# Kernel optimization log

Hardware: AMD Instinct MI355X
Metric: run time of the kernel (lower is better)

## Reference

```python
import jax, jax.numpy as jnp
import numpy as np

B, M, D = 8, 1024, 1024
H = 16
HD = D // H  # 64
F = 4096

def layer_norm(x, gamma, beta, eps=1e-5):
    mu = jnp.mean(x, axis=-1, keepdims=True)
    var = jnp.var(x, axis=-1, keepdims=True)
    return (x - mu) * jax.lax.rsqrt(var + eps) * gamma + beta

def setup_inputs() -> dict:
    key = jax.random.key(0)
    ks = jax.random.split(key, 16)
    s = 0.02
    return {
        "h": jax.random.normal(ks[0], (B, M, D), jnp.float32),
        "h_all": jax.random.normal(ks[1], (B, M, D), jnp.float32),
        "Wq": jax.random.normal(ks[2], (D, D), jnp.float32) * s,
        "Wk": jax.random.normal(ks[3], (D, D), jnp.float32) * s,
        "Wv": jax.random.normal(ks[4], (D, D), jnp.float32) * s,
        "Wo": jax.random.normal(ks[5], (D, D), jnp.float32) * s,
        "W1": jax.random.normal(ks[6], (D, F), jnp.float32) * s,
        "b1": jnp.zeros((F,), jnp.float32),
        "W2": jax.random.normal(ks[7], (F, D), jnp.float32) * s,
        "b2": jnp.zeros((D,), jnp.float32),
        "g1": jnp.ones((D,), jnp.float32),
        "be1": jnp.zeros((D,), jnp.float32),
        "g2": jnp.ones((D,), jnp.float32),
        "be2": jnp.zeros((D,), jnp.float32),
    }

def reference(h, h_all, Wq, Wk, Wv, Wo, W1, b1, W2, b2, g1, be1, g2, be2):
    Bx, Mx, Dx = h.shape
    # projections (no bias, per nn.Linear(bias=False))
    q = (h @ Wq).reshape(Bx, Mx, H, HD)        # [B,M,H,hd]
    k = (h_all @ Wk).reshape(Bx, -1, H, HD)    # [B,N,H,hd]
    v = (h_all @ Wv).reshape(Bx, -1, H, HD)
    # attention: scale by sqrt(head_dim) as in SeqAttention(hidden_size=head_dim)
    scores = jnp.einsum('bqhd,bkhd->bhqk', q, k) / jnp.sqrt(jnp.float32(HD))
    attn = jax.nn.softmax(scores, axis=-1)
    ctx = jnp.einsum('bhqk,bkhd->bqhd', attn, v).reshape(Bx, Mx, Dx)
    attn_out = ctx @ Wo
    # post-norm residual 1
    h1 = layer_norm(h + attn_out, g1, be1)
    # FFN
    ff = jax.nn.relu(h1 @ W1 + b1) @ W2 + b2
    # post-norm residual 2
    out = layer_norm(h1 + ff, g2, be2)
    return out
```

## Files before the change

kernel.cpp:

```cpp
#include <hip/hip_runtime.h>
#include <hip/hip_bf16.h>

#define ROWS 8192
#define DD   1024
#define HH   16
#define HD   64
#define FF   4096

typedef __attribute__((ext_vector_type(4))) float f32x4;
typedef __attribute__((ext_vector_type(8))) __bf16 bf16x8;

static __device__ __forceinline__ unsigned short f2bf(float f) {
  unsigned u = __float_as_uint(f);
  u += 0x7fffu + ((u >> 16) & 1u);
  return (unsigned short)(u >> 16);
}

static __device__ __forceinline__ float bf2f(unsigned short u) {
  return __uint_as_float(((unsigned)u) << 16);
}

static __device__ __forceinline__ unsigned cvtpk_bf16(float lo, float hi) {
  unsigned r;
  asm("v_cvt_pk_bf16_f32 %0, %1, %2" : "=v"(r) : "v"(lo), "v"(hi));
  return r;
}

static __device__ __forceinline__ f32x4 mfma16(bf16x8 a, bf16x8 b, f32x4 c) {
  return __builtin_amdgcn_mfma_f32_16x16x32_bf16(a, b, c, 0, 0, 0);
}

#define GLOAD16(gp, lp) __builtin_amdgcn_global_load_lds( \
    (__attribute__((address_space(1))) void*)(gp), \
    (__attribute__((address_space(3))) void*)(lp), 16, 0, 0)

__global__ __launch_bounds__(256) void prep_k(
    const float* __restrict__ h, const float* __restrict__ hall,
    const float* __restrict__ Wq, const float* __restrict__ Wk,
    const float* __restrict__ Wv, const float* __restrict__ Wo,
    const float* __restrict__ W1, const float* __restrict__ W2,
    unsigned short* __restrict__ hb, unsigned short* __restrict__ hab,
    unsigned short* __restrict__ wqt, unsigned short* __restrict__ wkvt,
    unsigned short* __restrict__ wot, unsigned short* __restrict__ w1t,
    unsigned short* __restrict__ w2t) {
  __shared__ float tile[32][33];
  const int bid = blockIdx.x;
  const int tid = threadIdx.x;

  if (bid < 16384) {
    const float* src = (bid < 8192) ? h : hall;
    unsigned short* dst = (bid < 8192) ? hb : hab;
    int i = (bid & 8191) * 256 + tid;
    float4 v = ((const float4*)src)[i];
    ushort4 o;
    o.x = f2bf(v.x); o.y = f2bf(v.y); o.z = f2bf(v.z); o.w = f2bf(v.w);
    ((ushort4*)dst)[i] = o;
    return;
  }

  int r = bid - 16384;
  const float* src; unsigned short* dst; int R, C, bx, by;
  if (r < 4096) {
    int which = r >> 10, idx = r & 1023;
    R = C = 1024; bx = idx & 31; by = idx >> 5;
    if (which == 0) { src = Wq; dst = wqt; }
    else if (which == 1) { src = Wk; dst = wkvt; }
    else if (which == 2) { src = Wv; dst = wkvt + (size_t)DD * DD; }
    else { src = Wo; dst = wot; }
  } else if (r < 8192) {
    int idx = r - 4096;
    R = 1024; C = 4096; bx = idx & 127; by = idx >> 7;
    src = W1; dst = w1t;
  } else {
    int idx = r - 8192;
    R = 4096; C = 1024; bx = idx & 31; by = idx >> 5;
    src = W2; dst = w2t;
  }
  const int tx = tid & 31, ty = tid >> 5;
  #pragma unroll
  for (int i = 0; i < 32; i += 8)
    tile[ty + i][tx] = src[(size_t)(by * 32 + ty + i) * C + bx * 32 + tx];
  __syncthreads();
  #pragma unroll
  for (int i = 0; i < 32; i += 8)
    dst[(size_t)(bx * 32 + ty + i) * R + by * 32 + tx] = f2bf(tile[tx][ty + i]);
}

template <int BM, int MODE, int KS = 1>
__global__ __launch_bounds__(512, 2) void gemm256(
    const unsigned short* __restrict__ A, const unsigned short* __restrict__ BT,
    const float* __restrict__ bias, void* __restrict__ Cout, void* __restrict__ Cout2,
    int Ni, int Ki, int nbx) {
  constexpr int MR = BM / 32;

  const int tid  = threadIdx.x;
  const int lane = tid & 63;
  const int wid  = tid >> 6;
  const int wm   = wid >> 2;
  const int wn   = wid & 3;
  const int lr   = lane & 15;
  const int kq   = lane >> 4;
  const int axor = (lr & 7) << 4;

  const int nwg = gridDim.x;
  const int cpx = nwg >> 3;
  const int wg  = (int)blockIdx.x;
  const int swz = (wg & 7) * cpx + (wg >> 3);
  const int perk = nwg / KS;
  const int kh   = swz / perk;
  const int swzr = swz % perk;
  const int bx = swzr % nbx, by = swzr / nbx;
  const int brow = by * BM, bcol = bx * 256;
  const int Kc   = Ki / KS;
  const int kbase = kh * Kc;

  f32x4 acc[MR][4] = {};
  const int NT = Kc >> 6;

  if constexpr (BM == 256) {
    __shared__ unsigned short As[2 * 256 * 64];
    __shared__ unsigned short Bs[2 * 256 * 64];

    const size_t loff = (size_t)(lane >> 3) * Ki + ((lane & 7) ^ (lane >> 3)) * 8;
    const unsigned short* Ab = A + (size_t)brow * Ki + kbase;
    const unsigned short* Bb = BT + (size_t)bcol * Ki + kbase;

    auto stage2 = [&](int qc, int u, int db) {
      const int ra = ((wid & 4) << 5) + qc * 32 + (wid & 3) * 8;
      GLOAD16(Ab + (size_t)ra * Ki + u * 64 + loff,
              (char*)As + db * 32768 + ra * 128);
      const int rb = qc * 64 + wid * 8;
      GLOAD16(Bb + (size_t)rb * Ki + u * 64 + loff,
              (char*)Bs + db * 32768 + rb * 128);
    };

    #pragma unroll
    for (int qc = 0; qc < 4; ++qc) stage2(qc, 0, 0);
    {
      const int u1 = (1 < NT) ? 1 : NT - 1;
      stage2(0, u1, 1); stage2(1, u1, 1); stage2(2, u1, 1);
    }
    asm volatile("s_waitcnt vmcnt(6)" ::: "memory");
    __builtin_amdgcn_s_barrier();
    __builtin_amdgcn_sched_barrier(0);

    #pragma unroll 1
    for (int t = 0; t < NT; ++t) {
      const int d = t & 1;
      const char* ab = (const char*)As + d * 32768;
      const char* bb = (const char*)Bs + d * 32768;
      bf16x8 bfv[4][2];
      #pragma unroll
      for (int q = 0; q < 4; ++q) {
        bf16x8 af[2][2];
        #pragma unroll
        for (int mm = 0; mm < 2; ++mm)
          #pragma unroll
          for (int ks = 0; ks < 2; ++ks)
            af[mm][ks] = *(const bf16x8*)(ab +
                (wm * 128 + (q * 2 + mm) * 16 + lr) * 128 +
                ((ks * 64 + kq * 16) ^ axor));
        if (q == 0) {
          #pragma unroll
          for (int n = 0; n < 4; ++n)
            #pragma unroll
            for (int ks = 0; ks < 2; ++ks)
              bfv[n][ks] = *(const bf16x8*)(bb +
                  (wn * 64 + n * 16 + lr) * 128 +
                  ((ks * 64 + kq * 16) ^ axor));
        }
        if (q == 0) {
          stage2(3, (t + 1 < NT) ? t + 1 : NT - 1, (t + 1) & 1);
        } else {
          stage2(q - 1, (t + 2 < NT) ? t + 2 : NT - 1, d);
        }
        __builtin_amdgcn_s_setprio(1);
        #pragma unroll
        for (int mm = 0; mm < 2; ++mm)
          #pragma unroll
          for (int n = 0; n < 4; ++n) {
            acc[q * 2 + mm][n] = mfma16(af[mm][0], bfv[n][0], acc[q * 2 + mm][n]);
            acc[q * 2 + mm][n] = mfma16(af[mm][1], bfv[n][1], acc[q * 2 + mm][n]);
          }
        __builtin_amdgcn_s_setprio(0);
        __builtin_amdgcn_sched_barrier(0);
        if (q == 3) asm volatile("s_waitcnt vmcnt(6)" ::: "memory");
        __builtin_amdgcn_s_barrier();
        __builtin_amdgcn_sched_barrier(0);
      }
    }
    asm volatile("s_waitcnt vmcnt(0)" ::: "memory");
  } else {
    __shared__ unsigned short As[2][BM * 64];
    __shared__ unsigned short Bs[2][256 * 64];
    const int srow = wid * 8 + (lane >> 3);
    const int scol = ((lane & 7) * 8) ^ ((srow & 7) << 3);
    size_t offA[BM / 64], offB[4];
    #pragma unroll
    for (int L = 0; L < BM / 64; ++L)
      offA[L] = (size_t)(brow + L * 64 + srow) * Ki + kbase + scol;
    #pragma unroll
    for (int L = 0; L < 4; ++L)
      offB[L] = (size_t)(bcol + L * 64 + srow) * Ki + kbase + scol;

    auto stage = [&](int t, int d) {
      #pragma unroll
      for (int L = 0; L < BM / 64; ++L)
        GLOAD16(A + offA[L] + t * 64, (char*)As[d] + L * 8192 + wid * 1024);
      #pragma unroll
      for (int L = 0; L < 4; ++L)
        GLOAD16(BT + offB[L] + t * 64, (char*)Bs[d] + L * 8192 + wid * 1024);
    };

    stage(0, 0);
    stage(1, 1);

    #pragma unroll 1
    for (int t = 0; t < NT; ++t) {
      const int d = t & 1;
      asm volatile("s_waitcnt vmcnt(6)" ::: "memory");
      __builtin_amdgcn_s_barrier();
      __builtin_amdgcn_sched_barrier(0);

      const unsigned short* as = As[d];
      const unsigned short* bs = Bs[d];
      #pragma unroll
      for (int kk = 0; kk < 2; ++kk) {
        bf16x8 af[MR], bfv[4];
        #pragma unroll
        for (int m = 0; m < MR; ++m)
          af[m] = *(const bf16x8*)((const char*)as +
              (wm * (BM / 2) + m * 16 + lr) * 128 + ((kk * 64 + kq * 16) ^ axor));
        #pragma unroll
        for (int n = 0; n < 4; ++n)
          bfv[n] = *(const bf16x8*)((const char*)bs +
              (wn * 64 + n * 16 + lr) * 128 + ((kk * 64 + kq * 16) ^ axor));
        #pragma unroll
        for (int m = 0; m < MR; ++m)
          #pragma unroll
          for (int n = 0; n < 4; ++n)
            acc[m][n] = mfma16(af[m], bfv[n], acc[m][n]);
      }

      asm volatile("s_waitcnt lgkmcnt(0)" ::: "memory");
      __builtin_amdgcn_s_barrier();
      __builtin_amdgcn_sched_barrier(0);
      const int ts = (t + 2 < NT) ? t + 2 : NT - 1;
      stage(ts, d);
    }
  }

  #pragma unroll
  for (int m = 0; m < MR; ++m) {
    #pragma unroll
    for (int n = 0; n < 4; ++n) {
      const int r0 = brow + wm * (BM / 2) + m * 16 + kq * 4;
      const int c  = bcol + wn * 64 + n * 16 + lr;
      if constexpr (MODE == 4) {
        if (c < 1024) {
          #pragma unroll
          for (int e = 0; e < 4; ++e)
            ((unsigned short*)Cout)[(size_t)(r0 + e) * 1024 + c] = f2bf(acc[m][n][e]);
        } else {
          const int cc = c - 1024;
          const int bq = r0 >> 10;
          const int tok = r0 & 1023;
          ushort4 pk;
          pk.x = f2bf(acc[m][n][0]); pk.y = f2bf(acc[m][n][1]);
          pk.z = f2bf(acc[m][n][2]); pk.w = f2bf(acc[m][n][3]);
          *(ushort4*)((unsigned short*)Cout2 + ((size_t)bq * 1024 + cc) * 1024 + tok) = pk;
        }
      } else if constexpr (MODE == 5) {
        unsigned short* o = (kh == 0) ? (unsigned short*)Cout : (unsigned short*)Cout2;
        #pragma unroll
        for (int e = 0; e < 4; ++e)
          o[(size_t)(r0 + e) * Ni + c] = f2bf(acc[m][n][e]);
      } else {
        const float bv = (MODE == 2 || MODE == 3) ? bias[c] : 0.0f;
        #pragma unroll
        for (int e = 0; e < 4; ++e) {
          float v = acc[m][n][e] + bv;
          if (MODE == 2) v = fmaxf(v, 0.0f);
          if (MODE == 0 || MODE == 2)
            ((unsigned short*)Cout)[(size_t)(r0 + e) * Ni + c] = f2bf(v);
          else
            ((float*)Cout)[(size_t)(r0 + e) * Ni + c] = v;
        }
      }
    }
  }
}

__global__ __launch_bounds__(512, 6) void attn_k(
    const unsigned short* __restrict__ q, const unsigned short* __restrict__ k,
    const unsigned short* __restrict__ vT, unsigned short* __restrict__ ctx) {
  __shared__ unsigned short Ks[2][64 * 64];
  __shared__ unsigned short Vt[2][64 * 64];
  __shared__ unsigned short Ps[8][16 * 64];
  const int tid = threadIdx.x;
  const int lane = tid & 63;
  const int wid = tid >> 6;
  const int bh = blockIdx.x;
  const int b = bh >> 4, h = bh & 15;
  const int qrow0 = blockIdx.y * 128 + wid * 16;
  const size_t tokbase = (size_t)b * 1024;
  const int lr = lane & 15, kq = lane >> 4;

  const int srow = tid >> 3;
  const int scol = ((tid & 7) * 8) ^ ((srow & 7) << 3);
  const unsigned short* kg = k + (tokbase + srow) * 1024 + h * 64 + scol;
  const unsigned short* vg = vT + ((size_t)(b * 16 + h) * 64 + srow) * 1024 + scol;
  const int ldst = tid * 16;

  auto stage = [&](int kt, int d) {
    GLOAD16(kg + (size_t)kt * 64 * 1024, (char*)Ks[d] + ldst);
    GLOAD16(vg + kt * 64, (char*)Vt[d] + ldst);
  };

  bf16x8 aq[2];
  {
    const unsigned short* qp = q + (tokbase + qrow0 + lr) * DD + h * 64 + kq * 8;
    aq[0] = *(const bf16x8*)qp;
    aq[1] = *(const bf16x8*)(qp + 32);
  }

  float l_acc = 0.f;
  f32x4 acc[4] = {};
  const float C = 0.125f * 1.4426950408889634f;
  const unsigned swp = (unsigned)((lr & 7) << 4);
  const unsigned pbase = (unsigned)(lr * 128);

  stage(0, 0);
  stage(1, 1);

  #pragma unroll 2
  for (int kt = 0; kt < 16; ++kt) {
    const int d = kt & 1;
    asm volatile("s_waitcnt vmcnt(2)" ::: "memory");
    __builtin_amdgcn_s_barrier();
    __builtin_amdgcn_sched_barrier(0);

    f32x4 sv[4] = {};
    __builtin_amdgcn_s_setprio(1);
    #pragma unroll
    for (int jb = 0; jb < 4; ++jb)
      #pragma unroll
      for (int ks = 0; ks < 2; ++ks) {
        int row = jb * 16 + lr;
        bf16x8 ak = *(const bf16x8*)((const char*)Ks[d] +
            row * 128 + ((ks * 64 + kq * 16) ^ ((row & 7) << 4)));
        sv[jb] = mfma16(ak, aq[ks], sv[jb]);
      }
    __builtin_amdgcn_s_setprio(0);

    #pragma unroll
    for (int jb = 0; jb < 4; ++jb) {
      float p0 = exp2f(sv[jb][0] * C);
      float p1 = exp2f(sv[jb][1] * C);
      float p2 = exp2f(sv[jb][2] * C);
      float p3 = exp2f(sv[jb][3] * C);
      l_acc += (p0 + p1) + (p2 + p3);
      uint2 w;
      w.x = cvtpk_bf16(p0, p1);
      w.y = cvtpk_bf16(p2, p3);
      unsigned off = pbase + (((unsigned)(jb * 32 + kq * 8)) ^ swp);
      *(uint2*)((char*)Ps[wid] + off) = w;
    }

    __builtin_amdgcn_s_setprio(1);
    #pragma unroll
    for (int ks = 0; ks < 2; ++ks) {
      bf16x8 ap = *(const bf16x8*)((const char*)Ps[wid] +
          lr * 128 + ((ks * 64 + kq * 16) ^ ((lr & 7) << 4)));
      #pragma unroll
      for (int db = 0; db < 4; ++db) {
        int dd = db * 16 + lr;
        bf16x8 bv = *(const bf16x8*)((const char*)Vt[d] +
            dd * 128 + ((ks * 64 + kq * 16) ^ ((dd & 7) << 4)));
        acc[db] = mfma16(bv, ap, acc[db]);
      }
    }
    __builtin_amdgcn_s_setprio(0);

    asm volatile("s_waitcnt lgkmcnt(0)" ::: "memory");
    __builtin_amdgcn_s_barrier();
    __builtin_amdgcn_sched_barrier(0);
    const int ts = (kt + 2 < 16) ? kt + 2 : 15;
    stage(ts, d);
  }

  float l = l_acc + __shfl_xor(l_acc, 16);
  l += __shfl_xor(l, 32);
  const float inv = 1.0f / l;
  unsigned short* cp = ctx + (tokbase + qrow0 + lr) * DD + h * 64 + kq * 4;
  #pragma unroll
  for (int db = 0; db < 4; ++db) {
    ushort4 o;
    o.x = f2bf(acc[db][0] * inv);
    o.y = f2bf(acc[db][1] * inv);
    o.z = f2bf(acc[db][2] * inv);
    o.w = f2bf(acc[db][3] * inv);
    *(ushort4*)(cp + db * 16) = o;
  }
}

__global__ __launch_bounds__(256) void ln_add_bb_k(
    const unsigned short* __restrict__ a, const unsigned short* __restrict__ b,
    const float* __restrict__ gamma, const float* __restrict__ beta,
    unsigned short* __restrict__ outb) {
  int row = blockIdx.x;
  int tid = threadIdx.x;
  size_t base = (size_t)row * 1024 + tid * 4;
  ushort4 va = *(const ushort4*)(a + base);
  ushort4 vb = *(const ushort4*)(b + base);
  float x[4] = {bf2f(va.x) + bf2f(vb.x), bf2f(va.y) + bf2f(vb.y),
                bf2f(va.z) + bf2f(vb.z), bf2f(va.w) + bf2f(vb.w)};
  float s = x[0] + x[1] + x[2] + x[3];
  float sq = x[0] * x[0] + x[1] * x[1] + x[2] * x[2] + x[3] * x[3];
  #pragma unroll
  for (int mk = 1; mk < 64; mk <<= 1) {
    s += __shfl_xor(s, mk);
    sq += __shfl_xor(sq, mk);
  }
  __shared__ float red[8];
  int wid = tid >> 6, lane = tid & 63;
  if (lane == 0) { red[wid] = s; red[4 + wid] = sq; }
  __syncthreads();
  s = red[0] + red[1] + red[2] + red[3];
  sq = red[4] + red[5] + red[6] + red[7];
  float mu = s * (1.0f / 1024.0f);
  float var = sq * (1.0f / 1024.0f) - mu * mu;
  float rs = rsqrtf(var + 1e-5f);
  float4 g = *(const float4*)(gamma + tid * 4);
  float4 be = *(const float4*)(beta + tid * 4);
  ushort4 ob;
  ob.x = f2bf((x[0] - mu) * rs * g.x + be.x);
  ob.y = f2bf((x[1] - mu) * rs * g.y + be.y);
  ob.z = f2bf((x[2] - mu) * rs * g.z + be.z);
  ob.w = f2bf((x[3] - mu) * rs * g.w + be.w);
  *(ushort4*)(outb + base) = ob;
}

__global__ __launch_bounds__(256) void ln3_k(
    const unsigned short* __restrict__ a, const unsigned short* __restrict__ p0,
    const unsigned short* __restrict__ p1, const float* __restrict__ b2,
    const float* __restrict__ gamma, const float* __restrict__ beta,
    float* __restrict__ outf) {
  int row = blockIdx.x;
  int tid = threadIdx.x;
  size_t base = (size_t)row * 1024 + tid * 4;
  ushort4 va = *(const ushort4*)(a + base);
  ushort4 v0 = *(const ushort4*)(p0 + base);
  ushort4 v1 = *(const ushort4*)(p1 + base);
  float4 bb = *(const float4*)(b2 + tid * 4);
  float x[4] = {bf2f(va.x) + bf2f(v0.x) + bf2f(v1.x) + bb.x,
                bf2f(va.y) + bf2f(v0.y) + bf2f(v1.y) + bb.y,
                bf2f(va.z) + bf2f(v0.z) + bf2f(v1.z) + bb.z,
                bf2f(va.w) + bf2f(v0.w) + bf2f(v1.w) + bb.w};
  float s = x[0] + x[1] + x[2] + x[3];
  float sq = x[0] * x[0] + x[1] * x[1] + x[2] * x[2] + x[3] * x[3];
  #pragma unroll
  for (int mk = 1; mk < 64; mk <<= 1) {
    s += __shfl_xor(s, mk);
    sq += __shfl_xor(sq, mk);
  }
  __shared__ float red[8];
  int wid = tid >> 6, lane = tid & 63;
  if (lane == 0) { red[wid] = s; red[4 + wid] = sq; }
  __syncthreads();
  s = red[0] + red[1] + red[2] + red[3];
  sq = red[4] + red[5] + red[6] + red[7];
  float mu = s * (1.0f / 1024.0f);
  float var = sq * (1.0f / 1024.0f) - mu * mu;
  float rs = rsqrtf(var + 1e-5f);
  float4 g = *(const float4*)(gamma + tid * 4);
  float4 be = *(const float4*)(beta + tid * 4);
  float4 o;
  o.x = (x[0] - mu) * rs * g.x + be.x;
  o.y = (x[1] - mu) * rs * g.y + be.y;
  o.z = (x[2] - mu) * rs * g.z + be.z;
  o.w = (x[3] - mu) * rs * g.w + be.w;
  *(float4*)(outf + base) = o;
}

extern "C" void kernel_launch(void* const* d_in, const int* in_sizes, int n_in,
                              void* d_out, int out_size, void* d_ws, size_t ws_size,
                              hipStream_t stream) {
  const float* h    = (const float*)d_in[0];
  const float* hall = (const float*)d_in[1];
  const float* Wq   = (const float*)d_in[2];
  const float* Wk   = (const float*)d_in[3];
  const float* Wv   = (const float*)d_in[4];
  const float* Wo   = (const float*)d_in[5];
  const float* W1   = (const float*)d_in[6];
  const float* b1   = (const float*)d_in[7];
  const float* W2   = (const float*)d_in[8];
  const float* b2   = (const float*)d_in[9];
  const float* g1   = (const float*)d_in[10];
  const float* be1  = (const float*)d_in[11];
  const float* g2   = (const float*)d_in[12];
  const float* be2  = (const float*)d_in[13];

  char* ws = (char*)d_ws;
  size_t off = 0;
  auto alloc = [&](size_t n) { size_t o = off; off += (n + 255) & ~(size_t)255; return o; };
  const size_t hb_o   = alloc((size_t)ROWS * DD * 2);
  const size_t hab_o  = alloc((size_t)ROWS * DD * 2);
  const size_t wqt_o  = alloc((size_t)DD * DD * 2);
  const size_t wkvt_o = alloc((size_t)DD * DD * 4);
  const size_t wot_o  = alloc((size_t)DD * DD * 2);
  const size_t w1t_o  = alloc((size_t)DD * FF * 2);
  const size_t w2t_o  = alloc((size_t)FF * DD * 2);
  const size_t qb_o   = alloc((size_t)ROWS * DD * 2);
  const size_t kb_o   = alloc((size_t)ROWS * DD * 2);
  const size_t vt_o   = alloc((size_t)ROWS * DD * 2);
  const size_t cx_o   = alloc((size_t)ROWS * DD * 2);
  const size_t h1b_o  = alloc((size_t)ROWS * DD * 2);
  const size_t fp1_o  = alloc((size_t)ROWS * DD * 2);

  unsigned short* hb   = (unsigned short*)(ws + hb_o);
  unsigned short* hab  = (unsigned short*)(ws + hab_o);
  unsigned short* wqt  = (unsigned short*)(ws + wqt_o);
  unsigned short* wkvt = (unsigned short*)(ws + wkvt_o);
  unsigned short* wot  = (unsigned short*)(ws + wot_o);
  unsigned short* w1t  = (unsigned short*)(ws + w1t_o);
  unsigned short* w2t  = (unsigned short*)(ws + w2t_o);
  unsigned short* qb   = (unsigned short*)(ws + qb_o);
  unsigned short* kb   = (unsigned short*)(ws + kb_o);
  unsigned short* vTb  = (unsigned short*)(ws + vt_o);
  unsigned short* cxb  = (unsigned short*)(ws + cx_o);
  unsigned short* h1b  = (unsigned short*)(ws + h1b_o);
  unsigned short* fp1b = (unsigned short*)(ws + fp1_o);
  unsigned short* attn_ob = (unsigned short*)(ws + hab_o);
  unsigned short* fp0b    = (unsigned short*)(ws + hb_o);
  unsigned short* ff1     = (unsigned short*)(ws + qb_o);
  float*          outf    = (float*)d_out;

  prep_k<<<dim3(16384 + 4096 + 4096 + 4096), 256, 0, stream>>>(
      h, hall, Wq, Wk, Wv, Wo, W1, W2, hb, hab, wqt, wkvt, wot, w1t, w2t);

  gemm256<128, 0><<<dim3(256), 512, 0, stream>>>(hb,  wqt,  nullptr, qb, nullptr, DD,   DD, 4);
  gemm256<256, 4><<<dim3(256), 512, 0, stream>>>(hab, wkvt, nullptr, kb, vTb,    2048, DD, 8);

  attn_k<<<dim3(128, 8), 512, 0, stream>>>(qb, kb, vTb, cxb);

  gemm256<128, 0><<<dim3(256), 512, 0, stream>>>(cxb, wot, nullptr, attn_ob, nullptr, DD, DD, 4);
  ln_add_bb_k<<<ROWS, 256, 0, stream>>>(hb, attn_ob, g1, be1, h1b);

  gemm256<256, 2>   <<<dim3(512), 512, 0, stream>>>(h1b, w1t, b1, ff1, nullptr, FF, DD, 16);
  gemm256<256, 5, 2><<<dim3(256), 512, 0, stream>>>(ff1, w2t, nullptr, fp0b, fp1b, DD, FF, 4);

  ln3_k<<<ROWS, 256, 0, stream>>>(h1b, fp0b, fp1b, b2, g2, be2, outf);
}
```

Baseline: 342.9 us.

## Merge Q and KV projection GEMMs into one launch and widen transpose tiles

The Q projection and the fused K/V projection GEMMs now run as a single 512-block launch. The GEMM body is factored into a device function that takes the LDS buffers and the block index as arguments, so the two GEMMs of different shapes share one kernel and fill the GPU together instead of running back to back. Separately, the weight-transpose prep now uses 64x64 tiles, converting to bf16 before the data goes to shared memory, which means fewer blocks and a smaller LDS footprint per element. The merged kernel reserves a full 128KB of LDS for every block, including the BM=128 ones, and the wider tiles change the store pattern.

```diff
diff --git a/kernel.cpp b/kernel.cpp
--- a/kernel.cpp
+++ b/kernel.cpp
@@ -43,7 +43,7 @@
     unsigned short* __restrict__ wqt, unsigned short* __restrict__ wkvt,
     unsigned short* __restrict__ wot, unsigned short* __restrict__ w1t,
     unsigned short* __restrict__ w2t) {
-  __shared__ float tile[32][33];
+  __shared__ unsigned short tile[64][66];
   const int bid = blockIdx.x;
   const int tid = threadIdx.x;
 
@@ -60,37 +60,42 @@
 
   int r = bid - 16384;
   const float* src; unsigned short* dst; int R, C, bx, by;
-  if (r < 4096) {
-    int which = r >> 10, idx = r & 1023;
-    R = C = 1024; bx = idx & 31; by = idx >> 5;
+  if (r < 1024) {
+    int which = r >> 8, idx = r & 255;
+    R = C = 1024; bx = idx & 15; by = idx >> 4;
     if (which == 0) { src = Wq; dst = wqt; }
     else if (which == 1) { src = Wk; dst = wkvt; }
     else if (which == 2) { src = Wv; dst = wkvt + (size_t)DD * DD; }
     else { src = Wo; dst = wot; }
-  } else if (r < 8192) {
-    int idx = r - 4096;
-    R = 1024; C = 4096; bx = idx & 127; by = idx >> 7;
+  } else if (r < 2048) {
+    int idx = r - 1024;
+    R = 1024; C = 4096; bx = idx & 63; by = idx >> 6;
     src = W1; dst = w1t;
   } else {
-    int idx = r - 8192;
-    R = 4096; C = 1024; bx = idx & 31; by = idx >> 5;
+    int idx = r - 2048;
+    R = 4096; C = 1024; bx = idx & 15; by = idx >> 4;
     src = W2; dst = w2t;
   }
-  const int tx = tid & 31, ty = tid >> 5;
+  const int col = tid & 63, q4 = tid >> 6;
   #pragma unroll
-  for (int i = 0; i < 32; i += 8)
-    tile[ty + i][tx] = src[(size_t)(by * 32 + ty + i) * C + bx * 32 + tx];
+  for (int i = 0; i < 16; ++i) {
+    int rr = q4 + i * 4;
+    tile[rr][col] = f2bf(src[(size_t)(by * 64 + rr) * C + bx * 64 + col]);
+  }
   __syncthreads();
   #pragma unroll
-  for (int i = 0; i < 32; i += 8)
-    dst[(size_t)(bx * 32 + ty + i) * R + by * 32 + tx] = f2bf(tile[tx][ty + i]);
+  for (int i = 0; i < 16; ++i) {
+    int c = q4 + i * 4;
+    dst[(size_t)(bx * 64 + c) * R + by * 64 + col] = tile[col][c];
+  }
 }
 
 template <int BM, int MODE, int KS = 1>
-__global__ __launch_bounds__(512, 2) void gemm256(
+static __device__ __forceinline__ void gemm_body(
+    char* ldsA, char* ldsB,
     const unsigned short* __restrict__ A, const unsigned short* __restrict__ BT,
     const float* __restrict__ bias, void* __restrict__ Cout, void* __restrict__ Cout2,
-    int Ni, int Ki, int nbx) {
+    int Ni, int Ki, int nbx, int wg, int nwg) {
   constexpr int MR = BM / 32;
 
   const int tid  = threadIdx.x;
@@ -102,9 +107,7 @@
   const int kq   = lane >> 4;
   const int axor = (lr & 7) << 4;
 
-  const int nwg = gridDim.x;
   const int cpx = nwg >> 3;
-  const int wg  = (int)blockIdx.x;
   const int swz = (wg & 7) * cpx + (wg >> 3);
   const int perk = nwg / KS;
   const int kh   = swz / perk;
@@ -118,20 +121,15 @@
   const int NT = Kc >> 6;
 
   if constexpr (BM == 256) {
-    __shared__ unsigned short As[2 * 256 * 64];
-    __shared__ unsigned short Bs[2 * 256 * 64];
-
     const size_t loff = (size_t)(lane >> 3) * Ki + ((lane & 7) ^ (lane >> 3)) * 8;
     const unsigned short* Ab = A + (size_t)brow * Ki + kbase;
     const unsigned short* Bb = BT + (size_t)bcol * Ki + kbase;
 
     auto stage2 = [&](int qc, int u, int db) {
       const int ra = ((wid & 4) << 5) + qc * 32 + (wid & 3) * 8;
-      GLOAD16(Ab + (size_t)ra * Ki + u * 64 + loff,
-              (char*)As + db * 32768 + ra * 128);
+      GLOAD16(Ab + (size_t)ra * Ki + u * 64 + loff, ldsA + db * 32768 + ra * 128);
       const int rb = qc * 64 + wid * 8;
-      GLOAD16(Bb + (size_t)rb * Ki + u * 64 + loff,
-              (char*)Bs + db * 32768 + rb * 128);
+      GLOAD16(Bb + (size_t)rb * Ki + u * 64 + loff, ldsB + db * 32768 + rb * 128);
     };
 
     #pragma unroll
@@ -147,8 +145,8 @@
     #pragma unroll 1
     for (int t = 0; t < NT; ++t) {
       const int d = t & 1;
-      const char* ab = (const char*)As + d * 32768;
-      const char* bb = (const char*)Bs + d * 32768;
+      const char* ab = ldsA + d * 32768;
+      const char* bb = ldsB + d * 32768;
       bf16x8 bfv[4][2];
       #pragma unroll
       for (int q = 0; q < 4; ++q) {
@@ -191,8 +189,6 @@
     }
     asm volatile("s_waitcnt vmcnt(0)" ::: "memory");
   } else {
-    __shared__ unsigned short As[2][BM * 64];
-    __shared__ unsigned short Bs[2][256 * 64];
     const int srow = wid * 8 + (lane >> 3);
     const int scol = ((lane & 7) * 8) ^ ((srow & 7) << 3);
     size_t offA[BM / 64], offB[4];
@@ -206,10 +202,10 @@
     auto stage = [&](int t, int d) {
       #pragma unroll
       for (int L = 0; L < BM / 64; ++L)
-        GLOAD16(A + offA[L] + t * 64, (char*)As[d] + L * 8192 + wid * 1024);
+        GLOAD16(A + offA[L] + t * 64, ldsA + d * (BM * 128) + L * 8192 + wid * 1024);
       #pragma unroll
       for (int L = 0; L < 4; ++L)
-        GLOAD16(BT + offB[L] + t * 64, (char*)Bs[d] + L * 8192 + wid * 1024);
+        GLOAD16(BT + offB[L] + t * 64, ldsB + d * 32768 + L * 8192 + wid * 1024);
     };
 
     stage(0, 0);
@@ -222,18 +218,18 @@
       __builtin_amdgcn_s_barrier();
       __builtin_amdgcn_sched_barrier(0);
 
-      const unsigned short* as = As[d];
-      const unsigned short* bs = Bs[d];
+      const char* as = ldsA + d * (BM * 128);
+      const char* bs = ldsB + d * 32768;
       #pragma unroll
       for (int kk = 0; kk < 2; ++kk) {
         bf16x8 af[MR], bfv[4];
         #pragma unroll
         for (int m = 0; m < MR; ++m)
-          af[m] = *(const bf16x8*)((const char*)as +
+          af[m] = *(const bf16x8*)(as +
               (wm * (BM / 2) + m * 16 + lr) * 128 + ((kk * 64 + kq * 16) ^ axor));
         #pragma unroll
         for (int n = 0; n < 4; ++n)
-          bfv[n] = *(const bf16x8*)((const char*)bs +
+          bfv[n] = *(const bf16x8*)(bs +
               (wn * 64 + n * 16 + lr) * 128 + ((kk * 64 + kq * 16) ^ axor));
         #pragma unroll
         for (int m = 0; m < MR; ++m)
@@ -289,6 +285,31 @@
       }
     }
   }
+}
+
+template <int BM, int MODE, int KS = 1>
+__global__ __launch_bounds__(512, 2) void gemm256(
+    const unsigned short* __restrict__ A, const unsigned short* __restrict__ BT,
+    const float* __restrict__ bias, void* __restrict__ Cout, void* __restrict__ Cout2,
+    int Ni, int Ki, int nbx) {
+  constexpr int ABYTES = 2 * BM * 64 * 2;
+  __shared__ char lds[ABYTES + 65536];
+  gemm_body<BM, MODE, KS>(lds, lds + ABYTES, A, BT, bias, Cout, Cout2,
+                          Ni, Ki, nbx, (int)blockIdx.x, (int)gridDim.x);
+}
+
+__global__ __launch_bounds__(512, 2) void qkv_k(
+    const unsigned short* __restrict__ hb, const unsigned short* __restrict__ hab,
+    const unsigned short* __restrict__ wqt, const unsigned short* __restrict__ wkvt,
+    unsigned short* __restrict__ qb, unsigned short* __restrict__ kb,
+    unsigned short* __restrict__ vTb) {
+  __shared__ char lds[131072];
+  if (blockIdx.x < 256)
+    gemm_body<256, 4, 1>(lds, lds + 65536, hab, wkvt, nullptr, kb, vTb,
+                         2048, 1024, 8, (int)blockIdx.x, 256);
+  else
+    gemm_body<128, 0, 1>(lds, lds + 32768, hb, wqt, nullptr, qb, nullptr,
+                         1024, 1024, 4, (int)blockIdx.x - 256, 256);
 }
 
 __global__ __launch_bounds__(512, 6) void attn_k(
@@ -536,11 +557,10 @@
   unsigned short* ff1     = (unsigned short*)(ws + qb_o);
   float*          outf    = (float*)d_out;
 
-  prep_k<<<dim3(16384 + 4096 + 4096 + 4096), 256, 0, stream>>>(
+  prep_k<<<dim3(16384 + 3072), 256, 0, stream>>>(
       h, hall, Wq, Wk, Wv, Wo, W1, W2, hb, hab, wqt, wkvt, wot, w1t, w2t);
 
-  gemm256<128, 0><<<dim3(256), 512, 0, stream>>>(hb,  wqt,  nullptr, qb, nullptr, DD,   DD, 4);
-  gemm256<256, 4><<<dim3(256), 512, 0, stream>>>(hab, wkvt, nullptr, kb, vTb,    2048, DD, 8);
+  qkv_k<<<dim3(512), 512, 0, stream>>>(hb, hab, wqt, wkvt, qb, kb, vTb);
 
   attn_k<<<dim3(128, 8), 512, 0, stream>>>(qb, kb, vTb, cxb);
 
```

Result: faster. 334.7 us, median of 4 (-2.4%).
